# Performance work log

Measured on AMD Instinct MI355X. Metric: run time of the kernel, lower is better.

## Reference

```python
import jax, jax.numpy as jnp
import numpy as np

B, S, D = 4, 4096, 1024
STATE = 1024
HID = 4 * D
EPS_NORM = 1e-6           # RMSNorm module eps
EPS_FP32 = 1.1920929e-7   # torch F.rms_norm default eps = finfo(fp32).eps


def rms_norm(x, eps):
    # no learned weight (RMSNorm(dim=-1) has weight=None)
    return x * jax.lax.rsqrt(jnp.mean(jnp.square(x), axis=-1, keepdims=True) + eps)


def setup_inputs() -> dict:
    key = jax.random.key(0)
    ks = jax.random.split(key, 8)
    scale_d = 1.0 / np.sqrt(D)
    scale_s = 1.0 / np.sqrt(STATE)
    scale_h = 1.0 / np.sqrt(HID)
    return {
        "x": jax.random.normal(ks[0], (B, S, D), jnp.float32),
        "x0": jax.random.normal(ks[1], (B, S, D), jnp.float32),
        "Wu": jax.random.normal(ks[2], (STATE, D), jnp.float32) * scale_d,
        "Wg": jax.random.normal(ks[3], (STATE, D), jnp.float32) * scale_d,
        "Wo": jax.random.normal(ks[4], (D, STATE), jnp.float32) * scale_s,
        "Wfc": jax.random.normal(ks[5], (HID, D), jnp.float32) * scale_d,
        "Wproj": jax.random.normal(ks[6], (D, HID), jnp.float32) * scale_h,
        "memory_mix": jnp.ones((D,), jnp.float32),
        "mlp_scale": jnp.ones((D,), jnp.float32),
        "resid_mix": jnp.stack([jnp.ones((D,), jnp.float32), jnp.zeros((D,), jnp.float32)]),
    }


def reference(x, x0, Wu, Wg, Wo, Wfc, Wproj, memory_mix, mlp_scale, resid_mix):
    # residual mix of x and x0
    x = resid_mix[0][None, None, :] * x + resid_mix[1][None, None, :] * x0

    # --- CausalPrefixMemory branch ---
    h = rms_norm(x, EPS_NORM)
    update = jnp.einsum('bsd,kd->bsk', h, Wu)
    gate = jax.nn.sigmoid(jnp.einsum('bsd,kd->bsk', h, Wg))
    memory = jnp.cumsum(gate * update, axis=1)          # [B,S,STATE]
    denom = jnp.arange(1, S + 1, dtype=jnp.float32)[None, :, None]
    m = rms_norm(memory / denom, EPS_FP32)
    mem_out = jnp.einsum('bsk,dk->bsd', m, Wo)
    x = x + memory_mix[None, None, :] * mem_out

    # --- MLP branch: relu^2 ---
    h2 = rms_norm(x, EPS_NORM)
    r = jax.nn.relu(jnp.einsum('bsd,hd->bsh', h2, Wfc))
    mlp_out = jnp.einsum('bsh,dh->bsd', jnp.square(r), Wproj)
    x = x + mlp_scale[None, None, :] * mlp_out
    return x
```

## Files before the change

### kernel.cpp

```cpp
#include <hip/hip_runtime.h>
#include <stdint.h>

typedef unsigned short u16;
typedef __attribute__((ext_vector_type(8))) short s16x8;
typedef __attribute__((ext_vector_type(4))) float f32x4;

__device__ __forceinline__ u16 f2bf(float f) {
  uint32_t u = __float_as_uint(f);
  uint32_t r = (u + 0x7FFFu + ((u >> 16) & 1u)) >> 16;
  return (u16)r;
}

__device__ __forceinline__ void gll16(const void* g, void* lds) {
  __builtin_amdgcn_global_load_lds(
      (const __attribute__((address_space(1))) uint32_t*)g,
      (__attribute__((address_space(3))) uint32_t*)lds, 16, 0, 0);
}

__device__ __forceinline__ void xcd_swz(int& bx, int& by) {
  int gx = gridDim.x;
  int lin = blockIdx.y * gx + blockIdx.x;
  int cpx = (gx * gridDim.y) >> 3;
  int nl = (lin & 7) * cpx + (lin >> 3);
  bx = nl % gx;
  by = nl / gx;
}

__global__ __launch_bounds__(256) void k_f2b(const float* __restrict__ src,
                                             u16* __restrict__ dst, int n) {
  int i = (blockIdx.x * 256 + threadIdx.x) * 4;
  if (i < n) {
    float4 v = *(const float4*)(src + i);
    ushort4 o;
    o.x = f2bf(v.x); o.y = f2bf(v.y); o.z = f2bf(v.z); o.w = f2bf(v.w);
    *(ushort4*)(dst + i) = o;
  }
}

template <bool MIX>
__global__ __launch_bounds__(256) void k_rms(const float* __restrict__ X,
                                             const float* __restrict__ X0,
                                             const float* __restrict__ rmix,
                                             float* __restrict__ XMout,
                                             u16* __restrict__ Hout, float eps) {
  const int row = blockIdx.x, t = threadIdx.x;
  const size_t base = (size_t)row * 1024;
  float4 v;
  if (MIX) {
    float4 a = ((const float4*)(X + base))[t];
    float4 b = ((const float4*)(X0 + base))[t];
    float4 c0 = ((const float4*)rmix)[t];
    float4 c1 = ((const float4*)(rmix + 1024))[t];
    v.x = c0.x * a.x + c1.x * b.x;
    v.y = c0.y * a.y + c1.y * b.y;
    v.z = c0.z * a.z + c1.z * b.z;
    v.w = c0.w * a.w + c1.w * b.w;
  } else {
    v = ((const float4*)(X + base))[t];
  }
  float ss = v.x * v.x + v.y * v.y + v.z * v.z + v.w * v.w;
#pragma unroll
  for (int o = 32; o > 0; o >>= 1) ss += __shfl_xor(ss, o);
  __shared__ float red[4];
  if ((t & 63) == 0) red[t >> 6] = ss;
  __syncthreads();
  float tot = red[0] + red[1] + red[2] + red[3];
  float sc = rsqrtf(tot * (1.0f / 1024.0f) + eps);
  if (MIX) ((float4*)(XMout + base))[t] = v;
  ushort4 hv;
  hv.x = f2bf(v.x * sc); hv.y = f2bf(v.y * sc);
  hv.z = f2bf(v.z * sc); hv.w = f2bf(v.w * sc);
  ((ushort4*)(Hout + base))[t] = hv;
}

__global__ __launch_bounds__(256) void k_rms_mem(const float* __restrict__ Mem,
                                                 u16* __restrict__ Mout) {
  const int row = blockIdx.x, t = threadIdx.x;
  const float inv = 1.0f / (float)((row & 4095) + 1);
  const size_t base = (size_t)row * 1024;
  float4 v = ((const float4*)(Mem + base))[t];
  v.x *= inv; v.y *= inv; v.z *= inv; v.w *= inv;
  float ss = v.x * v.x + v.y * v.y + v.z * v.z + v.w * v.w;
#pragma unroll
  for (int o = 32; o > 0; o >>= 1) ss += __shfl_xor(ss, o);
  __shared__ float red[4];
  if ((t & 63) == 0) red[t >> 6] = ss;
  __syncthreads();
  float tot = red[0] + red[1] + red[2] + red[3];
  float sc = rsqrtf(tot * (1.0f / 1024.0f) + 1.1920929e-7f);
  ushort4 hv;
  hv.x = f2bf(v.x * sc); hv.y = f2bf(v.y * sc);
  hv.z = f2bf(v.z * sc); hv.w = f2bf(v.w * sc);
  ((ushort4*)(Mout + base))[t] = hv;
}

__global__ __launch_bounds__(256) void k_scan1(const float* __restrict__ P,
                                               float* __restrict__ CS) {
  int blk = blockIdx.x;
  int chunk = blk & 63, b = blk >> 6;
  const float4* p = (const float4*)(P + ((size_t)b * 4096 + chunk * 64) * 1024)
                    + threadIdx.x;
  float4 s = {0.f, 0.f, 0.f, 0.f};
#pragma unroll 8
  for (int i = 0; i < 64; ++i) {
    float4 v = p[(size_t)i * 256];
    s.x += v.x; s.y += v.y; s.z += v.z; s.w += v.w;
  }
  ((float4*)(CS + ((size_t)b * 64 + chunk) * 1024))[threadIdx.x] = s;
}

__global__ __launch_bounds__(256) void k_scan2(float* __restrict__ CS) {
  int idx = blockIdx.x * 256 + threadIdx.x;
  int b = idx >> 10, k = idx & 1023;
  float run = 0.f;
  for (int c = 0; c < 64; ++c) {
    size_t o = ((size_t)b * 64 + c) * 1024 + k;
    float v = CS[o];
    CS[o] = run;
    run += v;
  }
}

__global__ __launch_bounds__(256) void k_scan3(float* __restrict__ P,
                                               const float* __restrict__ CS) {
  int blk = blockIdx.x;
  int chunk = blk & 63, b = blk >> 6;
  float4 run = ((const float4*)(CS + ((size_t)b * 64 + chunk) * 1024))[threadIdx.x];
  float4* p = (float4*)(P + ((size_t)b * 4096 + chunk * 64) * 1024) + threadIdx.x;
#pragma unroll 8
  for (int i = 0; i < 64; ++i) {
    float4 v = p[(size_t)i * 256];
    run.x += v.x; run.y += v.y; run.z += v.z; run.w += v.w;
    p[(size_t)i * 256] = run;
  }
}

__global__ __launch_bounds__(256, 2) void gemm_dual(
    const u16* __restrict__ A, const u16* __restrict__ Bu,
    const u16* __restrict__ Bg, float* __restrict__ P, int K) {
  __shared__ __align__(16) u16 As[128 * 64];
  __shared__ __align__(16) u16 Us[64 * 64];
  __shared__ __align__(16) u16 Gs[64 * 64];
  const int t = threadIdx.x;
  const int lane = t & 63, wid = t >> 6;
  int bx, by;
  xcd_swz(bx, by);
  const int m0 = by * 128, n0 = bx * 64;
  const int wm = wid * 32;
  const int l15 = lane & 15, lhi = lane >> 4;

  size_t gA[4], gU[2];
#pragma unroll
  for (int i = 0; i < 4; ++i) {
    int j = i * 256 + t;
    int row = j >> 3;
    int k16 = (j & 7) ^ (row & 7);
    gA[i] = (size_t)(m0 + row) * K + k16 * 8;
  }
#pragma unroll
  for (int i = 0; i < 2; ++i) {
    int j = i * 256 + t;
    int row = j >> 3;
    int k16 = (j & 7) ^ (row & 7);
    gU[i] = (size_t)(n0 + row) * K + k16 * 8;
  }

  f32x4 au[2][4], ag[2][4];
#pragma unroll
  for (int mi = 0; mi < 2; ++mi)
#pragma unroll
    for (int ni = 0; ni < 4; ++ni) { au[mi][ni] = 0.0f; ag[mi][ni] = 0.0f; }

  for (int kb = 0; kb < K; kb += 64) {
#pragma unroll
    for (int i = 0; i < 4; ++i) {
      int j = i * 256 + t;
      gll16(A + gA[i] + kb, &As[j * 8]);
    }
#pragma unroll
    for (int i = 0; i < 2; ++i) {
      int j = i * 256 + t;
      gll16(Bu + gU[i] + kb, &Us[j * 8]);
      gll16(Bg + gU[i] + kb, &Gs[j * 8]);
    }
    __syncthreads();
#pragma unroll
    for (int kc = 0; kc < 2; ++kc) {
      s16x8 af[2], uf[4], gf[4];
#pragma unroll
      for (int mi = 0; mi < 2; ++mi) {
        int row = wm + mi * 16 + l15;
        int k16 = (kc * 4 + lhi) ^ (row & 7);
        af[mi] = *(const s16x8*)&As[row * 64 + k16 * 8];
      }
#pragma unroll
      for (int ni = 0; ni < 4; ++ni) {
        int row = ni * 16 + l15;
        int k16 = (kc * 4 + lhi) ^ (row & 7);
        uf[ni] = *(const s16x8*)&Us[row * 64 + k16 * 8];
        gf[ni] = *(const s16x8*)&Gs[row * 64 + k16 * 8];
      }
#pragma unroll
      for (int mi = 0; mi < 2; ++mi)
#pragma unroll
        for (int ni = 0; ni < 4; ++ni) {
          au[mi][ni] = __builtin_amdgcn_mfma_f32_16x16x32_bf16(
              af[mi], uf[ni], au[mi][ni], 0, 0, 0);
          ag[mi][ni] = __builtin_amdgcn_mfma_f32_16x16x32_bf16(
              af[mi], gf[ni], ag[mi][ni], 0, 0, 0);
        }
    }
    __syncthreads();
  }

#pragma unroll
  for (int mi = 0; mi < 2; ++mi) {
    int r0 = m0 + wm + mi * 16 + lhi * 4;
#pragma unroll
    for (int ni = 0; ni < 4; ++ni) {
      int c = n0 + ni * 16 + l15;
#pragma unroll
      for (int j = 0; j < 4; ++j) {
        float u = au[mi][ni][j], g = ag[mi][ni][j];
        P[(size_t)(r0 + j) * 1024 + c] = u / (1.0f + __expf(-g));
      }
    }
  }
}

template <int EPI>
__global__ __launch_bounds__(256, 2) void gemm_bf16(
    const u16* __restrict__ A, const u16* __restrict__ Bw, void* __restrict__ Cout,
    const float* __restrict__ Cadd, const float* __restrict__ colscale,
    int K, int lda, int ldb, int ldc) {
  __shared__ __align__(16) u16 As[128 * 64];
  __shared__ __align__(16) u16 Bs[128 * 64];
  const int t = threadIdx.x;
  const int lane = t & 63, wid = t >> 6;
  int bx, by;
  xcd_swz(bx, by);
  const int m0 = by * 128, n0 = bx * 128;
  const int wm = (wid >> 1) * 64, wn = (wid & 1) * 64;
  const int l15 = lane & 15, lhi = lane >> 4;

  size_t gA[4], gB[4];
#pragma unroll
  for (int i = 0; i < 4; ++i) {
    int j = i * 256 + t;
    int row = j >> 3;
    int k16 = (j & 7) ^ (row & 7);
    gA[i] = (size_t)(m0 + row) * lda + k16 * 8;
    gB[i] = (size_t)(n0 + row) * ldb + k16 * 8;
  }

  f32x4 acc[4][4];
#pragma unroll
  for (int mi = 0; mi < 4; ++mi)
#pragma unroll
    for (int ni = 0; ni < 4; ++ni) acc[mi][ni] = 0.0f;

  for (int kb = 0; kb < K; kb += 64) {
#pragma unroll
    for (int i = 0; i < 4; ++i) {
      int j = i * 256 + t;
      gll16(A + gA[i] + kb, &As[j * 8]);
      gll16(Bw + gB[i] + kb, &Bs[j * 8]);
    }
    __syncthreads();
#pragma unroll
    for (int kc = 0; kc < 2; ++kc) {
      s16x8 af[4], bfr[4];
#pragma unroll
      for (int mi = 0; mi < 4; ++mi) {
        int row = wm + mi * 16 + l15;
        int k16 = (kc * 4 + lhi) ^ (row & 7);
        af[mi] = *(const s16x8*)&As[row * 64 + k16 * 8];
      }
#pragma unroll
      for (int ni = 0; ni < 4; ++ni) {
        int row = wn + ni * 16 + l15;
        int k16 = (kc * 4 + lhi) ^ (row & 7);
        bfr[ni] = *(const s16x8*)&Bs[row * 64 + k16 * 8];
      }
#pragma unroll
      for (int mi = 0; mi < 4; ++mi)
#pragma unroll
        for (int ni = 0; ni < 4; ++ni)
          acc[mi][ni] = __builtin_amdgcn_mfma_f32_16x16x32_bf16(
              af[mi], bfr[ni], acc[mi][ni], 0, 0, 0);
    }
    __syncthreads();
  }

#pragma unroll
  for (int mi = 0; mi < 4; ++mi) {
    int r0 = m0 + wm + mi * 16 + lhi * 4;
#pragma unroll
    for (int ni = 0; ni < 4; ++ni) {
      int c = n0 + wn + ni * 16 + l15;
      float cs = (EPI == 1) ? colscale[c] : 0.f;
#pragma unroll
      for (int j = 0; j < 4; ++j) {
        size_t idx = (size_t)(r0 + j) * ldc + c;
        float v = acc[mi][ni][j];
        if (EPI == 1) {
          ((float*)Cout)[idx] = Cadd[idx] + cs * v;
        } else {
          float rv = fmaxf(v, 0.f);
          ((u16*)Cout)[idx] = f2bf(rv * rv);
        }
      }
    }
  }
}

extern "C" void kernel_launch(void* const* d_in, const int* in_sizes, int n_in,
                              void* d_out, int out_size, void* d_ws, size_t ws_size,
                              hipStream_t stream) {
  const float* x = (const float*)d_in[0];
  const float* x0 = (const float*)d_in[1];
  const float* Wu = (const float*)d_in[2];
  const float* Wg = (const float*)d_in[3];
  const float* Wo = (const float*)d_in[4];
  const float* Wfc = (const float*)d_in[5];
  const float* Wpj = (const float*)d_in[6];
  const float* mmix = (const float*)d_in[7];
  const float* mscale = (const float*)d_in[8];
  const float* rmix = (const float*)d_in[9];
  float* out = (float*)d_out;

  const int M = 16384;
  const size_t MiB = 1024 * 1024;

  char* ws = (char*)d_ws;
  u16* WuB = (u16*)ws;   ws += 2 * MiB;
  u16* WgB = (u16*)ws;   ws += 2 * MiB;
  u16* WoB = (u16*)ws;   ws += 2 * MiB;
  u16* WfcB = (u16*)ws;  ws += 8 * MiB;
  u16* WpjB = (u16*)ws;  ws += 8 * MiB;
  u16* h = (u16*)ws;     ws += 32 * MiB;
  char* pool = ws;
  float* P = (float*)pool;
  float* CS = (float*)(pool + 64 * MiB);
  u16* mB = (u16*)(pool + 65 * MiB);
  u16* R2 = (u16*)pool;
  float* xm = out;

  const bool fullR2 = ws_size >= 182 * MiB;

  k_f2b<<<1024, 256, 0, stream>>>(Wu, WuB, 1024 * 1024);
  k_f2b<<<1024, 256, 0, stream>>>(Wg, WgB, 1024 * 1024);
  k_f2b<<<1024, 256, 0, stream>>>(Wo, WoB, 1024 * 1024);
  k_f2b<<<4096, 256, 0, stream>>>(Wfc, WfcB, 4096 * 1024);
  k_f2b<<<4096, 256, 0, stream>>>(Wpj, WpjB, 4096 * 1024);

  k_rms<true><<<M, 256, 0, stream>>>(x, x0, rmix, xm, h, 1e-6f);

  gemm_dual<<<dim3(16, 128), 256, 0, stream>>>(h, WuB, WgB, P, 1024);

  k_scan1<<<256, 256, 0, stream>>>(P, CS);
  k_scan2<<<16, 256, 0, stream>>>(CS);
  k_scan3<<<256, 256, 0, stream>>>(P, CS);

  k_rms_mem<<<M, 256, 0, stream>>>(P, mB);

  gemm_bf16<1><<<dim3(8, 128), 256, 0, stream>>>(mB, WoB, xm, xm, mmix,
                                                 1024, 1024, 1024, 1024);
  k_rms<false><<<M, 256, 0, stream>>>(xm, nullptr, nullptr, nullptr, h, 1e-6f);

  if (fullR2) {
    for (int c = 0; c < 2; ++c)
      gemm_bf16<2><<<dim3(16, 128), 256, 0, stream>>>(
          h, WfcB + (size_t)c * 2048 * 1024, R2 + (size_t)c * 2048, nullptr,
          nullptr, 1024, 1024, 1024, 4096);
    gemm_bf16<1><<<dim3(8, 128), 256, 0, stream>>>(
        R2, WpjB, out, out, mscale, 4096, 4096, 4096, 1024);
  } else {
    for (int c = 0; c < 2; ++c) {
      gemm_bf16<2><<<dim3(16, 128), 256, 0, stream>>>(
          h, WfcB + (size_t)c * 2048 * 1024, R2, nullptr, nullptr,
          1024, 1024, 1024, 2048);
      gemm_bf16<1><<<dim3(8, 128), 256, 0, stream>>>(
          R2, WpjB + (size_t)c * 2048, out, out, mscale,
          2048, 2048, 4096, 1024);
    }
  }
}
```

Before: 525.8 us.

## Fuse scan third pass with memory RMSNorm and merge FC GEMM launches

The final prefix-scan pass now also divides by position, computes the row RMSNorm with a per-row block reduction, and writes bf16 directly. This removes the fp32 write-back of the cumulative memory and the separate normalisation kernel's full re-read. In exchange, each of the 64 rows per block needs a __syncthreads, and only 256 blocks run the fused work. Separately, the two half-width FC GEMM launches are merged into one launch over the full hidden width when the workspace is large enough.

```diff
diff --git a/kernel.cpp b/kernel.cpp
--- a/kernel.cpp
+++ b/kernel.cpp
@@ -73,27 +73,6 @@
   ((ushort4*)(Hout + base))[t] = hv;
 }
 
-__global__ __launch_bounds__(256) void k_rms_mem(const float* __restrict__ Mem,
-                                                 u16* __restrict__ Mout) {
-  const int row = blockIdx.x, t = threadIdx.x;
-  const float inv = 1.0f / (float)((row & 4095) + 1);
-  const size_t base = (size_t)row * 1024;
-  float4 v = ((const float4*)(Mem + base))[t];
-  v.x *= inv; v.y *= inv; v.z *= inv; v.w *= inv;
-  float ss = v.x * v.x + v.y * v.y + v.z * v.z + v.w * v.w;
-#pragma unroll
-  for (int o = 32; o > 0; o >>= 1) ss += __shfl_xor(ss, o);
-  __shared__ float red[4];
-  if ((t & 63) == 0) red[t >> 6] = ss;
-  __syncthreads();
-  float tot = red[0] + red[1] + red[2] + red[3];
-  float sc = rsqrtf(tot * (1.0f / 1024.0f) + 1.1920929e-7f);
-  ushort4 hv;
-  hv.x = f2bf(v.x * sc); hv.y = f2bf(v.y * sc);
-  hv.z = f2bf(v.z * sc); hv.w = f2bf(v.w * sc);
-  ((ushort4*)(Mout + base))[t] = hv;
-}
-
 __global__ __launch_bounds__(256) void k_scan1(const float* __restrict__ P,
                                                float* __restrict__ CS) {
   int blk = blockIdx.x;
@@ -121,17 +100,33 @@
   }
 }
 
-__global__ __launch_bounds__(256) void k_scan3(float* __restrict__ P,
-                                               const float* __restrict__ CS) {
+__global__ __launch_bounds__(256) void k_scan3f(const float* __restrict__ P,
+                                                const float* __restrict__ CS,
+                                                u16* __restrict__ Mout) {
   int blk = blockIdx.x;
   int chunk = blk & 63, b = blk >> 6;
-  float4 run = ((const float4*)(CS + ((size_t)b * 64 + chunk) * 1024))[threadIdx.x];
-  float4* p = (float4*)(P + ((size_t)b * 4096 + chunk * 64) * 1024) + threadIdx.x;
-#pragma unroll 8
+  const int t = threadIdx.x, wid = t >> 6;
+  __shared__ float red[2][4];
+  float4 run = ((const float4*)(CS + ((size_t)b * 64 + chunk) * 1024))[t];
+  const float4* p = (const float4*)(P + ((size_t)b * 4096 + chunk * 64) * 1024) + t;
+  u16* mo = Mout + ((size_t)b * 4096 + chunk * 64) * 1024 + t * 4;
   for (int i = 0; i < 64; ++i) {
     float4 v = p[(size_t)i * 256];
     run.x += v.x; run.y += v.y; run.z += v.z; run.w += v.w;
-    p[(size_t)i * 256] = run;
+    float inv = 1.0f / (float)(chunk * 64 + i + 1);
+    float4 y;
+    y.x = run.x * inv; y.y = run.y * inv; y.z = run.z * inv; y.w = run.w * inv;
+    float ss = y.x * y.x + y.y * y.y + y.z * y.z + y.w * y.w;
+#pragma unroll
+    for (int o = 32; o > 0; o >>= 1) ss += __shfl_xor(ss, o);
+    if ((t & 63) == 0) red[i & 1][wid] = ss;
+    __syncthreads();
+    float tot = red[i & 1][0] + red[i & 1][1] + red[i & 1][2] + red[i & 1][3];
+    float sc = rsqrtf(tot * (1.0f / 1024.0f) + 1.1920929e-7f);
+    ushort4 hv;
+    hv.x = f2bf(y.x * sc); hv.y = f2bf(y.y * sc);
+    hv.z = f2bf(y.z * sc); hv.w = f2bf(y.w * sc);
+    *(ushort4*)(mo + (size_t)i * 1024) = hv;
   }
 }
 
@@ -360,19 +355,15 @@
 
   k_scan1<<<256, 256, 0, stream>>>(P, CS);
   k_scan2<<<16, 256, 0, stream>>>(CS);
-  k_scan3<<<256, 256, 0, stream>>>(P, CS);
-
-  k_rms_mem<<<M, 256, 0, stream>>>(P, mB);
+  k_scan3f<<<256, 256, 0, stream>>>(P, CS, mB);
 
   gemm_bf16<1><<<dim3(8, 128), 256, 0, stream>>>(mB, WoB, xm, xm, mmix,
                                                  1024, 1024, 1024, 1024);
   k_rms<false><<<M, 256, 0, stream>>>(xm, nullptr, nullptr, nullptr, h, 1e-6f);
 
   if (fullR2) {
-    for (int c = 0; c < 2; ++c)
-      gemm_bf16<2><<<dim3(16, 128), 256, 0, stream>>>(
-          h, WfcB + (size_t)c * 2048 * 1024, R2 + (size_t)c * 2048, nullptr,
-          nullptr, 1024, 1024, 1024, 4096);
+    gemm_bf16<2><<<dim3(32, 128), 256, 0, stream>>>(
+        h, WfcB, R2, nullptr, nullptr, 1024, 1024, 1024, 4096);
     gemm_bf16<1><<<dim3(8, 128), 256, 0, stream>>>(
         R2, WpjB, out, out, mscale, 4096, 4096, 4096, 1024);
   } else {
```

New measurement: 532.2 us. About the same (+1.2%).
